# Optimization experiments

Hardware: AMD Instinct MI355X
Metric: run time of the kernel (lower is better)

The kernel has to match this reference:

```python
import jax, jax.numpy as jnp
import numpy as np
from jax import lax

N, CIN, COUT = 10000, 64, 32
RADIUS = 0.07
K = 32            # cap on neighbors per query (radius search truncated to K nearest)
KSIZE = 3         # kernel_size = [3,3,3]
NCELLS = KSIZE ** 3

# 8 trilinear corner offsets
_OFFS = np.array([[i, j, k] for i in (0, 1) for j in (0, 1) for k in (0, 1)], dtype=np.int32)  # (8,3)
_STRIDE = np.array([KSIZE * KSIZE, KSIZE, 1], dtype=np.int32)


def setup_inputs() -> dict:
    key = jax.random.key(0)
    k1, k2, k3 = jax.random.split(key, 3)
    points = jax.random.uniform(k1, (N, 3), dtype=jnp.float32)
    feats = jax.random.normal(k2, (N, CIN), dtype=jnp.float32)
    # ContinuousConv kernel: [3,3,3,Cin,Cout] flattened to [27,Cin,Cout]
    W = jax.random.normal(k3, (NCELLS, CIN, COUT), dtype=jnp.float32) * 0.05
    b = jnp.zeros((COUT,), dtype=jnp.float32)
    return {"feats": feats, "points": points, "W": W, "b": b}


def _neighbors(points):
    # squared pairwise distances (N,N); radius search truncated to K nearest
    sq = jnp.sum(points * points, axis=-1)
    d2 = sq[:, None] + sq[None, :] - 2.0 * (points @ points.T)
    neg_d2, idx = lax.top_k(-d2, K)           # (N,K)
    valid = (-neg_d2) <= RADIUS * RADIUS      # (N,K) bool
    return idx, valid


def _cconv(feats, points, W, b, idx, valid):
    nb_pos = points[idx]                      # (N,K,3) gather
    rel = (nb_pos - points[:, None, :]) / RADIUS   # normalized by half-extent -> unit ball
    # ball_to_cube_radial: v -> v * ||v||_2 / ||v||_inf  (0 at origin)
    l2 = jnp.linalg.norm(rel, axis=-1, keepdims=True)
    linf = jnp.max(jnp.abs(rel), axis=-1, keepdims=True)
    t = jnp.where(linf > 0, rel * (l2 / jnp.maximum(linf, 1e-12)), 0.0)  # in [-1,1]^3
    # map to kernel grid coords in [0, KSIZE-1]
    coords = (t + 1.0) * 0.5 * (KSIZE - 1)    # (N,K,3)
    c0 = jnp.clip(jnp.floor(coords), 0, KSIZE - 2)
    f = coords - c0                            # trilinear fractions, (N,K,3)
    offs = jnp.asarray(_OFFS)                  # (8,3)
    # trilinear weights (N,K,8)
    fw = jnp.where(offs[None, None] == 1, f[:, :, None, :], 1.0 - f[:, :, None, :])
    w8 = jnp.prod(fw, axis=-1)
    # flattened corner cell indices (N,K,8)
    cidx = jnp.sum((c0[:, :, None, :].astype(jnp.int32) + offs) * jnp.asarray(_STRIDE), axis=-1)
    onehot = jax.nn.one_hot(cidx, NCELLS, dtype=feats.dtype)        # (N,K,8,27)
    wmass = jnp.einsum('nke,nkej->nkj', w8, onehot)                 # (N,K,27)
    wmass = wmass * valid[:, :, None].astype(feats.dtype)
    nb_feats = feats[idx]                                           # (N,K,Cin)
    A = jnp.einsum('nkj,nkf->njf', wmass, nb_feats)                 # (N,27,Cin)
    out = jnp.einsum('njf,jfo->no', A, W)                           # (N,Cout)
    # normalize=True: divide by neighbor importance sum (count, window=None)
    nn = jnp.sum(valid.astype(feats.dtype), axis=-1)
    out = out / jnp.maximum(nn, 1.0)[:, None] + b
    return out


@jax.jit
def reference(feats, points, W, b):
    idx, valid = _neighbors(points)
    return _cconv(feats, points, W, b, idx, valid)
```

## Files before the change

kernel.cpp:

```cpp
#include <hip/hip_runtime.h>
#include <math.h>

#define N_PTS   10000
#define CIN     64
#define COUT    32
#define KCAP    32
#define RADIUSF 0.07f
#define NCELLS  27
#define QB      4
#define MAXC    48
#define GRES    14
#define GCELLS  (GRES * GRES * GRES)
#define CPAD    72
#define NBBLD   28
#define WT_ELEMS (NCELLS * COUT * CIN)

typedef __attribute__((ext_vector_type(8))) short         bf16x8_t;
typedef __attribute__((ext_vector_type(4))) float         f32x4_t;

__device__ __forceinline__ void cell_coords(float x, float y, float z,
                                            int& cx, int& cy, int& cz) {
    cx = (int)(x * (float)GRES); if (cx > GRES - 1) cx = GRES - 1; if (cx < 0) cx = 0;
    cy = (int)(y * (float)GRES); if (cy > GRES - 1) cy = GRES - 1; if (cy < 0) cy = 0;
    cz = (int)(z * (float)GRES); if (cz > GRES - 1) cz = GRES - 1; if (cz < 0) cz = 0;
}

__device__ __forceinline__ unsigned int f2bf_u(float x) {
    unsigned int u = __float_as_uint(x);
    return (u + 0x7FFFu + ((u >> 16) & 1u)) >> 16;
}

__global__ __launch_bounds__(1024) void build_rep_kernel(
    const float* __restrict__ pts,
    const float* __restrict__ W,
    int*   __restrict__ offsets,
    int*   __restrict__ sorted,
    int*   __restrict__ cursor,
    float* __restrict__ pts_s,
    unsigned short* __restrict__ Wt)
{
    __shared__ int   s_hist[GCELLS];
    __shared__ int   s_scan[1024];
    __shared__ float tile[CIN * 33];
    const int t = threadIdx.x;
    const int b = blockIdx.x;

    for (int i = t; i < GCELLS; i += 1024) s_hist[i] = 0;
    __syncthreads();
    for (int i = t; i < N_PTS; i += 1024) {
        int cx, cy, cz;
        cell_coords(pts[3 * i], pts[3 * i + 1], pts[3 * i + 2], cx, cy, cz);
        atomicAdd(&s_hist[(cx * GRES + cy) * GRES + cz], 1);
    }
    __syncthreads();

    const int c0 = t * 3;
    int v0 = (c0 + 0 < GCELLS) ? s_hist[c0 + 0] : 0;
    int v1 = (c0 + 1 < GCELLS) ? s_hist[c0 + 1] : 0;
    int v2 = (c0 + 2 < GCELLS) ? s_hist[c0 + 2] : 0;
    s_scan[t] = v0 + v1 + v2;
    __syncthreads();
    for (int d = 1; d < 1024; d <<= 1) {
        int add = (t >= d) ? s_scan[t - d] : 0;
        __syncthreads();
        s_scan[t] += add;
        __syncthreads();
    }
    int base = (t == 0) ? 0 : s_scan[t - 1];
    if (c0 + 0 < GCELLS) { s_hist[c0 + 0] = base; base += v0; }
    if (c0 + 1 < GCELLS) { s_hist[c0 + 1] = base; base += v1; }
    if (c0 + 2 < GCELLS) { s_hist[c0 + 2] = base; base += v2; }
    __syncthreads();

    if (b == 0) {
        for (int i = t; i < GCELLS; i += 1024) offsets[i] = s_hist[i];
        if (t == 0) offsets[GCELLS] = N_PTS;
    }

    const int per = (N_PTS + NBBLD - 1) / NBBLD;
    const int lo = b * per;
    const int hi = (lo + per < N_PTS) ? lo + per : N_PTS;
    for (int i = lo + t; i < hi; i += 1024) {
        float x = pts[3 * i + 0], y = pts[3 * i + 1], z = pts[3 * i + 2];
        int cx, cy, cz;
        cell_coords(x, y, z, cx, cy, cz);
        int cell = (cx * GRES + cy) * GRES + cz;
        int pos = s_hist[cell] + atomicAdd(&cursor[cell], 1);
        sorted[pos] = i;
        pts_s[3 * pos + 0] = x;
        pts_s[3 * pos + 1] = y;
        pts_s[3 * pos + 2] = z;
    }

    if (b >= 1) {
        const int cell = b - 1;
        __syncthreads();
        for (int idx = t; idx < CIN * COUT; idx += 1024) {
            int f = idx >> 5, o = idx & 31;
            tile[f * 33 + o] = W[cell * (CIN * COUT) + idx];
        }
        __syncthreads();
        for (int idx = t; idx < CIN * COUT; idx += 1024) {
            int o = idx >> 6, f = idx & 63;
            Wt[cell * (CIN * COUT) + idx] = (unsigned short)f2bf_u(tile[f * 33 + o]);
        }
    }
}

__global__ __launch_bounds__(256) void cconv_grid_mfma_kernel(
    const float* __restrict__ feats,
    const unsigned short* __restrict__ Wt,
    const float* __restrict__ bias,
    const int*   __restrict__ offsets,
    const int*   __restrict__ sorted,
    const float* __restrict__ pts_s,
    float* __restrict__ out)
{
    const int tid  = threadIdx.x;
    const int lane = tid & 63;
    const int wave = tid >> 6;

    __shared__ __align__(16) unsigned short sAb[QB][NCELLS][CPAD];
    __shared__ __align__(16) float s_pool[QB][4][MAXC];
    __shared__ int   s_idx[QB][MAXC];
    __shared__ int   s_sel[QB][KCAP];
    __shared__ int   s_cnt[QB];
    __shared__ int   s_qi[QB];
    __shared__ int   s_nn[QB];

    if (lane == 0) s_cnt[wave] = 0;

    const int q_flat = blockIdx.x * QB + wave;
    const int qi = sorted[q_flat];
    const float qx = pts_s[3 * q_flat + 0];
    const float qy = pts_s[3 * q_flat + 1];
    const float qz = pts_s[3 * q_flat + 2];
    const float sqn = qx * qx + qy * qy + qz * qz;
    const float r2 = RADIUSF * RADIUSF;

    int cx, cy, cz;
    cell_coords(qx, qy, qz, cx, cy, cz);

    int zlo = cz - 1; if (zlo < 0) zlo = 0;
    int zhi = cz + 1; if (zhi > GRES - 1) zhi = GRES - 1;
    int ss[9], sl[9];
    #pragma unroll
    for (int dxi = 0; dxi < 3; ++dxi) {
        #pragma unroll
        for (int dyi = 0; dyi < 3; ++dyi) {
            const int ii = dxi * 3 + dyi;
            int cxx = cx + dxi - 1, cyy = cy + dyi - 1;
            bool ok = (cxx >= 0) && (cxx <= GRES - 1) && (cyy >= 0) && (cyy <= GRES - 1);
            int row = ((ok ? cxx : 0) * GRES + (ok ? cyy : 0)) * GRES;
            int s = offsets[row + zlo];
            int e = offsets[row + zhi + 1];
            ss[ii] = s;
            sl[ii] = ok ? (e - s) : 0;
        }
    }
    int cum[10];
    cum[0] = 0;
    #pragma unroll
    for (int ii = 0; ii < 9; ++ii) cum[ii + 1] = cum[ii] + sl[ii];
    const int T = cum[9];

    for (int t = lane; t < T; t += 64) {
        int gidx = 0;
        #pragma unroll
        for (int ii = 0; ii < 9; ++ii) {
            bool in = (t >= cum[ii]) && (t < cum[ii + 1]);
            int cand = ss[ii] + (t - cum[ii]);
            gidx = in ? cand : gidx;
        }
        float x = pts_s[3 * gidx + 0];
        float y = pts_s[3 * gidx + 1];
        float z = pts_s[3 * gidx + 2];
        float sqj = x * x + y * y + z * z;
        float dot = qx * x + qy * y + qz * z;
        float d2 = (sqn + sqj) - 2.0f * dot;
        if (d2 <= r2) {
            int pos = atomicAdd(&s_cnt[wave], 1);
            if (pos < MAXC) {
                s_pool[wave][0][pos] = d2;
                s_pool[wave][1][pos] = x;
                s_pool[wave][2][pos] = y;
                s_pool[wave][3][pos] = z;
                s_idx[wave][pos] = sorted[gidx];
            }
        }
    }

    int M = s_cnt[wave]; if (M > MAXC) M = MAXC;
    const int cnt = (M > KCAP) ? KCAP : M;
    const bool over = (M > KCAP);

    if (over) {
        if (lane < M) {
            float dc = s_pool[wave][0][lane];
            int   ic = s_idx[wave][lane];
            int rank = 0;
            for (int m = 0; m < M; ++m) {
                float dm = s_pool[wave][0][m];
                int   im = s_idx[wave][m];
                rank += (dm < dc || (dm == dc && im < ic)) ? 1 : 0;
            }
            if (rank < KCAP) s_sel[wave][rank] = lane;
        }
    }
    if (lane == 0) { s_qi[wave] = qi; s_nn[wave] = cnt; }

    float* w9w = (float*)&sAb[wave][0][0];
    if (lane < cnt) {
        int slot = over ? s_sel[wave][lane] : lane;
        float x = s_pool[wave][1][slot];
        float y = s_pool[wave][2][slot];
        float z = s_pool[wave][3][slot];
        int   j = s_idx[wave][slot];
        float rx = (x - qx) / RADIUSF;
        float ry = (y - qy) / RADIUSF;
        float rz = (z - qz) / RADIUSF;
        float l2 = sqrtf(rx * rx + ry * ry + rz * rz);
        float ax = fabsf(rx), ay = fabsf(ry), az = fabsf(rz);
        float linf = fmaxf(fmaxf(ax, ay), az);
        float s = (linf > 0.0f) ? (l2 / fmaxf(linf, 1e-12f)) : 0.0f;
        float tx = rx * s, ty = ry * s, tz = rz * s;
        float cxf = (tx + 1.0f) * 0.5f * 2.0f;
        float cyf = (ty + 1.0f) * 0.5f * 2.0f;
        float czf = (tz + 1.0f) * 0.5f * 2.0f;
        float c0x = fminf(fmaxf(floorf(cxf), 0.0f), 1.0f);
        float c0y = fminf(fmaxf(floorf(cyf), 0.0f), 1.0f);
        float c0z = fminf(fmaxf(floorf(czf), 0.0f), 1.0f);
        float fx = cxf - c0x;
        float fy = cyf - c0y;
        float fz = czf - c0z;
        int i0 = (int)c0x, i1 = (int)c0y, i2 = (int)c0z;
        float gx0 = 1.0f - fx, gx1 = fx;
        float gy0 = 1.0f - fy, gy1 = fy;
        float gz0 = 1.0f - fz, gz1 = fz;
        float* wp = w9w + lane * 12;
        wp[0] = i0 ? 0.0f : gx0;  wp[1] = i0 ? gx0 : gx1;  wp[2] = i0 ? gx1 : 0.0f;
        wp[3] = i1 ? 0.0f : gy0;  wp[4] = i1 ? gy0 : gy1;  wp[5] = i1 ? gy1 : 0.0f;
        wp[6] = i2 ? 0.0f : gz0;  wp[7] = i2 ? gz0 : gz1;  wp[8] = i2 ? gz1 : 0.0f;
        wp[9] = __int_as_float(j * CIN);
    }

    float a[NCELLS];
    #pragma unroll
    for (int c = 0; c < NCELLS; ++c) a[c] = 0.0f;

    if (cnt > 0) {
        int jb = __float_as_int(w9w[9]);
        float fv = feats[jb + lane];
        for (int k = 0; k < cnt; ++k) {
            const float* wp = w9w + k * 12;
            float wxv[3] = {wp[0], wp[1], wp[2]};
            float wyv[3] = {wp[3], wp[4], wp[5]};
            float wz0 = wp[6], wz1 = wp[7], wz2 = wp[8];
            float fv_cur = fv;
            if (k + 1 < cnt) {
                int jb2 = __float_as_int(w9w[(k + 1) * 12 + 9]);
                fv = feats[jb2 + lane];
            }
            float pzv[3] = {wz0 * fv_cur, wz1 * fv_cur, wz2 * fv_cur};
            #pragma unroll
            for (int ci = 0; ci < 3; ++ci) {
                #pragma unroll
                for (int cj = 0; cj < 3; ++cj) {
                    float wxy = wxv[ci] * wyv[cj];
                    #pragma unroll
                    for (int ck = 0; ck < 3; ++ck) {
                        a[ci * 9 + cj * 3 + ck] = fmaf(wxy, pzv[ck], a[ci * 9 + cj * 3 + ck]);
                    }
                }
            }
        }
    }
    #pragma unroll
    for (int c = 0; c < NCELLS; ++c) sAb[wave][c][lane] = (unsigned short)f2bf_u(a[c]);
    __syncthreads();

    float (*sC)[QB][COUT] = (float (*)[QB][COUT])&s_pool[0][0][0];
    f32x4_t acc0 = {0.f, 0.f, 0.f, 0.f};
    f32x4_t acc1 = {0.f, 0.f, 0.f, 0.f};
    const int r  = lane & 15;
    const int kg = lane >> 4;
    for (int s = wave; s < 2 * NCELLS; s += QB) {
        const int c  = s >> 1;
        const int f0 = (s & 1) << 5;
        bf16x8_t af = {};
        if (r < QB) af = *(const bf16x8_t*)&sAb[r][c][f0 + kg * 8];
        const unsigned short* wp0 = Wt + ((c * COUT + r     ) * CIN + f0 + kg * 8);
        const unsigned short* wp1 = Wt + ((c * COUT + 16 + r) * CIN + f0 + kg * 8);
        bf16x8_t bf0 = *(const bf16x8_t*)wp0;
        bf16x8_t bf1 = *(const bf16x8_t*)wp1;
        acc0 = __builtin_amdgcn_mfma_f32_16x16x32_bf16(af, bf0, acc0, 0, 0, 0);
        acc1 = __builtin_amdgcn_mfma_f32_16x16x32_bf16(af, bf1, acc1, 0, 0, 0);
    }
    if (lane < 16) {
        #pragma unroll
        for (int j = 0; j < QB; ++j) {
            sC[wave][j][lane]      = acc0[j];
            sC[wave][j][16 + lane] = acc1[j];
        }
    }
    __syncthreads();

    if (tid < QB * COUT) {
        int q = tid >> 5, o = tid & 31;
        float v = sC[0][q][o] + sC[1][q][o] + sC[2][q][o] + sC[3][q][o];
        float nn = (float)s_nn[q];
        out[s_qi[q] * COUT + o] = v / fmaxf(nn, 1.0f) + bias[o];
    }
}

__global__ __launch_bounds__(64) void cconv_fused_kernel(
    const float* __restrict__ feats,
    const float* __restrict__ points,
    const float* __restrict__ W,
    const float* __restrict__ bias,
    float* __restrict__ out)
{
    const int n    = blockIdx.x;
    const int lane = threadIdx.x;

    __shared__ float sA[NCELLS][CIN];
    __shared__ float s_d2[128];
    __shared__ int   s_idx[128];
    __shared__ int   s_rank[128];
    __shared__ int   s_sel[KCAP];
    __shared__ int   s_cnt;

    if (lane == 0) s_cnt = 0;
    for (int c = lane; c < NCELLS * CIN; c += 64) ((float*)sA)[c] = 0.0f;
    __syncthreads();

    const float qx = points[3 * n + 0];
    const float qy = points[3 * n + 1];
    const float qz = points[3 * n + 2];
    const float sqn = qx * qx + qy * qy + qz * qz;
    const float r2 = RADIUSF * RADIUSF;

    for (int j = lane; j < N_PTS; j += 64) {
        float x = points[3 * j + 0];
        float y = points[3 * j + 1];
        float z = points[3 * j + 2];
        float sqj = x * x + y * y + z * z;
        float dot = qx * x + qy * y + qz * z;
        float d2 = (sqn + sqj) - 2.0f * dot;
        if (d2 <= r2) {
            int pos = atomicAdd(&s_cnt, 1);
            if (pos < 128) { s_d2[pos] = d2; s_idx[pos] = j; }
        }
    }
    __syncthreads();

    int M = s_cnt; if (M > 128) M = 128;
    int cnt;
    if (M > KCAP) {
        for (int c = lane; c < M; c += 64) {
            float dc = s_d2[c]; int ic = s_idx[c]; int rank = 0;
            for (int m = 0; m < M; ++m) {
                float dm = s_d2[m]; int im = s_idx[m];
                rank += (dm < dc || (dm == dc && im < ic)) ? 1 : 0;
            }
            s_rank[c] = rank;
        }
        __syncthreads();
        for (int c = lane; c < M; c += 64) {
            int r = s_rank[c];
            if (r < KCAP) s_sel[r] = s_idx[c];
        }
        __syncthreads();
        cnt = KCAP;
    } else cnt = M;
    const int* nbr = (M > KCAP) ? s_sel : s_idx;

    for (int k = 0; k < cnt; ++k) {
        int j = nbr[k];
        float x = points[3 * j + 0];
        float y = points[3 * j + 1];
        float z = points[3 * j + 2];
        float rx = (x - qx) / RADIUSF;
        float ry = (y - qy) / RADIUSF;
        float rz = (z - qz) / RADIUSF;
        float l2 = sqrtf(rx * rx + ry * ry + rz * rz);
        float ax = fabsf(rx), ay = fabsf(ry), az = fabsf(rz);
        float linf = fmaxf(fmaxf(ax, ay), az);
        float s = (linf > 0.0f) ? (l2 / fmaxf(linf, 1e-12f)) : 0.0f;
        float tx = rx * s, ty = ry * s, tz = rz * s;
        float cxf = (tx + 1.0f) * 0.5f * 2.0f;
        float cyf = (ty + 1.0f) * 0.5f * 2.0f;
        float czf = (tz + 1.0f) * 0.5f * 2.0f;
        float c0x = fminf(fmaxf(floorf(cxf), 0.0f), 1.0f);
        float c0y = fminf(fmaxf(floorf(cyf), 0.0f), 1.0f);
        float c0z = fminf(fmaxf(floorf(czf), 0.0f), 1.0f);
        float fx = cxf - c0x, fy = cyf - c0y, fz = czf - c0z;
        int i0 = (int)c0x, i1 = (int)c0y, i2 = (int)c0z;
        int base = i0 * 9 + i1 * 3 + i2;
        float gx0 = 1.0f - fx, gx1 = fx;
        float gy0 = 1.0f - fy, gy1 = fy;
        float gz0 = 1.0f - fz, gz1 = fz;
        float featv = feats[j * CIN + lane];
        sA[base + 0 ][lane] += (gx0 * gy0) * gz0 * featv;
        sA[base + 1 ][lane] += (gx0 * gy0) * gz1 * featv;
        sA[base + 3 ][lane] += (gx0 * gy1) * gz0 * featv;
        sA[base + 4 ][lane] += (gx0 * gy1) * gz1 * featv;
        sA[base + 9 ][lane] += (gx1 * gy0) * gz0 * featv;
        sA[base + 10][lane] += (gx1 * gy0) * gz1 * featv;
        sA[base + 12][lane] += (gx1 * gy1) * gz0 * featv;
        sA[base + 13][lane] += (gx1 * gy1) * gz1 * featv;
    }
    __syncthreads();

    const int o    = lane & 31;
    const int half = lane >> 5;
    const int c_begin = half ? 14 : 0;
    const int c_end   = half ? 27 : 14;
    float acc = 0.0f;
    for (int cell = c_begin; cell < c_end; ++cell) {
        const float* __restrict__ Wrow = W + (cell * CIN) * COUT + o;
        #pragma unroll 8
        for (int f = 0; f < CIN; ++f) acc += sA[cell][f] * Wrow[f * COUT];
    }
    acc += __shfl_xor(acc, 32);
    if (lane < COUT) {
        float nn = (float)cnt;
        out[n * COUT + lane] = acc / fmaxf(nn, 1.0f) + bias[lane];
    }
}

extern "C" void kernel_launch(void* const* d_in, const int* in_sizes, int n_in,
                              void* d_out, int out_size, void* d_ws, size_t ws_size,
                              hipStream_t stream) {
    const float* feats  = (const float*)d_in[0];
    const float* points = (const float*)d_in[1];
    const float* W      = (const float*)d_in[2];
    const float* bias   = (const float*)d_in[3];
    float* out = (float*)d_out;

    const size_t wt_bytes = (size_t)WT_ELEMS * sizeof(unsigned short);
    const size_t need     = wt_bytes
                          + (size_t)(GCELLS + 1 + N_PTS + GCELLS) * sizeof(int)
                          + (size_t)3 * N_PTS * sizeof(float);

    if (ws_size >= need) {
        unsigned short* Wt = (unsigned short*)d_ws;
        int* offsets = (int*)((char*)d_ws + wt_bytes);
        int* sorted  = offsets + GCELLS + 1;
        int* cursor  = sorted + N_PTS;
        float* pts_s = (float*)(cursor + GCELLS);

        hipMemsetAsync(cursor, 0, GCELLS * sizeof(int), stream);
        build_rep_kernel<<<NBBLD, 1024, 0, stream>>>(points, W, offsets, sorted, cursor, pts_s, Wt);
        cconv_grid_mfma_kernel<<<N_PTS / QB, QB * 64, 0, stream>>>(
            feats, Wt, bias, offsets, sorted, pts_s, out);
    } else {
        cconv_fused_kernel<<<N_PTS, 64, 0, stream>>>(feats, points, W, bias, out);
    }
}
```

Before: 120.8 us.

## Split grid build into single-block scan and scatter kernels; deepen feature prefetch

The redundant 28-block histogram-plus-scan becomes a single-block kernel with a wave-shuffle scan that writes the offsets and seeds the cursors. This removes the memset. A separate 256-thread kernel then does the point scatter across 40 blocks and the weight transpose across 27 blocks. In the conv kernel, the original-index lookup moves out of the candidate loop into a per-lane pass. Feature prefetch becomes two-deep, and the MFMA loop is fully unrolled to 14 iterations with a zero-padded extra cell row. This trades one extra kernel launch for less redundant work and serialization, and adds some shared memory.

```diff
diff --git a/kernel.cpp b/kernel.cpp
--- a/kernel.cpp
+++ b/kernel.cpp
@@ -12,7 +12,7 @@
 #define GRES    14
 #define GCELLS  (GRES * GRES * GRES)
 #define CPAD    72
-#define NBBLD   28
+#define NSCAT   40
 #define WT_ELEMS (NCELLS * COUT * CIN)
 
 typedef __attribute__((ext_vector_type(8))) short         bf16x8_t;
@@ -30,20 +30,16 @@
     return (u + 0x7FFFu + ((u >> 16) & 1u)) >> 16;
 }
 
-__global__ __launch_bounds__(1024) void build_rep_kernel(
+__global__ __launch_bounds__(1024) void k1_hist_scan(
     const float* __restrict__ pts,
-    const float* __restrict__ W,
-    int*   __restrict__ offsets,
-    int*   __restrict__ sorted,
-    int*   __restrict__ cursor,
-    float* __restrict__ pts_s,
-    unsigned short* __restrict__ Wt)
+    int* __restrict__ offsets,
+    int* __restrict__ cursor)
 {
-    __shared__ int   s_hist[GCELLS];
-    __shared__ int   s_scan[1024];
-    __shared__ float tile[CIN * 33];
+    __shared__ int s_hist[GCELLS];
+    __shared__ int s_wsum[16];
     const int t = threadIdx.x;
-    const int b = blockIdx.x;
+    const int lane = t & 63;
+    const int wv   = t >> 6;
 
     for (int i = t; i < GCELLS; i += 1024) s_hist[i] = 0;
     __syncthreads();
@@ -58,49 +54,63 @@
     int v0 = (c0 + 0 < GCELLS) ? s_hist[c0 + 0] : 0;
     int v1 = (c0 + 1 < GCELLS) ? s_hist[c0 + 1] : 0;
     int v2 = (c0 + 2 < GCELLS) ? s_hist[c0 + 2] : 0;
-    s_scan[t] = v0 + v1 + v2;
-    __syncthreads();
-    for (int d = 1; d < 1024; d <<= 1) {
-        int add = (t >= d) ? s_scan[t - d] : 0;
-        __syncthreads();
-        s_scan[t] += add;
-        __syncthreads();
-    }
-    int base = (t == 0) ? 0 : s_scan[t - 1];
-    if (c0 + 0 < GCELLS) { s_hist[c0 + 0] = base; base += v0; }
-    if (c0 + 1 < GCELLS) { s_hist[c0 + 1] = base; base += v1; }
-    if (c0 + 2 < GCELLS) { s_hist[c0 + 2] = base; base += v2; }
-    __syncthreads();
-
-    if (b == 0) {
-        for (int i = t; i < GCELLS; i += 1024) offsets[i] = s_hist[i];
-        if (t == 0) offsets[GCELLS] = N_PTS;
-    }
-
-    const int per = (N_PTS + NBBLD - 1) / NBBLD;
-    const int lo = b * per;
-    const int hi = (lo + per < N_PTS) ? lo + per : N_PTS;
-    for (int i = lo + t; i < hi; i += 1024) {
-        float x = pts[3 * i + 0], y = pts[3 * i + 1], z = pts[3 * i + 2];
-        int cx, cy, cz;
-        cell_coords(x, y, z, cx, cy, cz);
-        int cell = (cx * GRES + cy) * GRES + cz;
-        int pos = s_hist[cell] + atomicAdd(&cursor[cell], 1);
-        sorted[pos] = i;
-        pts_s[3 * pos + 0] = x;
-        pts_s[3 * pos + 1] = y;
-        pts_s[3 * pos + 2] = z;
-    }
-
-    if (b >= 1) {
-        const int cell = b - 1;
-        __syncthreads();
-        for (int idx = t; idx < CIN * COUT; idx += 1024) {
+    const int local = v0 + v1 + v2;
+    int inc = local;
+    #pragma unroll
+    for (int d = 1; d < 64; d <<= 1) {
+        int up = __shfl_up(inc, d);
+        if (lane >= d) inc += up;
+    }
+    if (lane == 63) s_wsum[wv] = inc;
+    __syncthreads();
+    if (t == 0) {
+        int run = 0;
+        #pragma unroll
+        for (int i = 0; i < 16; ++i) { int tmp = s_wsum[i]; s_wsum[i] = run; run += tmp; }
+    }
+    __syncthreads();
+    int base = s_wsum[wv] + (inc - local);
+    if (c0 + 0 < GCELLS) { offsets[c0 + 0] = base; cursor[c0 + 0] = base; base += v0; }
+    if (c0 + 1 < GCELLS) { offsets[c0 + 1] = base; cursor[c0 + 1] = base; base += v1; }
+    if (c0 + 2 < GCELLS) { offsets[c0 + 2] = base; cursor[c0 + 2] = base; base += v2; }
+    if (t == 0) offsets[GCELLS] = N_PTS;
+}
+
+__global__ __launch_bounds__(256) void k2_scatter_wt(
+    const float* __restrict__ pts,
+    const float* __restrict__ W,
+    int*   __restrict__ cursor,
+    int*   __restrict__ sorted,
+    float* __restrict__ pts_s,
+    unsigned short* __restrict__ Wt)
+{
+    const int b = blockIdx.x;
+    const int t = threadIdx.x;
+
+    if (b < NSCAT) {
+        const int per = N_PTS / NSCAT;
+        const int lo = b * per;
+        const int hi = lo + per;
+        for (int i = lo + t; i < hi; i += 256) {
+            float x = pts[3 * i + 0], y = pts[3 * i + 1], z = pts[3 * i + 2];
+            int cx, cy, cz;
+            cell_coords(x, y, z, cx, cy, cz);
+            int cell = (cx * GRES + cy) * GRES + cz;
+            int pos = atomicAdd(&cursor[cell], 1);
+            sorted[pos] = i;
+            pts_s[3 * pos + 0] = x;
+            pts_s[3 * pos + 1] = y;
+            pts_s[3 * pos + 2] = z;
+        }
+    } else {
+        __shared__ float tile[CIN * 33];
+        const int cell = b - NSCAT;
+        for (int idx = t; idx < CIN * COUT; idx += 256) {
             int f = idx >> 5, o = idx & 31;
             tile[f * 33 + o] = W[cell * (CIN * COUT) + idx];
         }
         __syncthreads();
-        for (int idx = t; idx < CIN * COUT; idx += 1024) {
+        for (int idx = t; idx < CIN * COUT; idx += 256) {
             int o = idx >> 6, f = idx & 63;
             Wt[cell * (CIN * COUT) + idx] = (unsigned short)f2bf_u(tile[f * 33 + o]);
         }
@@ -120,9 +130,10 @@
     const int lane = tid & 63;
     const int wave = tid >> 6;
 
-    __shared__ __align__(16) unsigned short sAb[QB][NCELLS][CPAD];
+    __shared__ __align__(16) unsigned short sAb[QB][NCELLS + 1][CPAD];
     __shared__ __align__(16) float s_pool[QB][4][MAXC];
     __shared__ int   s_idx[QB][MAXC];
+    __shared__ int   s_org[QB][MAXC];
     __shared__ int   s_sel[QB][KCAP];
     __shared__ int   s_cnt[QB];
     __shared__ int   s_qi[QB];
@@ -185,7 +196,7 @@
                 s_pool[wave][1][pos] = x;
                 s_pool[wave][2][pos] = y;
                 s_pool[wave][3][pos] = z;
-                s_idx[wave][pos] = sorted[gidx];
+                s_idx[wave][pos] = gidx;
             }
         }
     }
@@ -194,14 +205,16 @@
     const int cnt = (M > KCAP) ? KCAP : M;
     const bool over = (M > KCAP);
 
+    if (lane < M) s_org[wave][lane] = sorted[s_idx[wave][lane]];
+
     if (over) {
         if (lane < M) {
             float dc = s_pool[wave][0][lane];
-            int   ic = s_idx[wave][lane];
+            int   ic = s_org[wave][lane];
             int rank = 0;
             for (int m = 0; m < M; ++m) {
                 float dm = s_pool[wave][0][m];
-                int   im = s_idx[wave][m];
+                int   im = s_org[wave][m];
                 rank += (dm < dc || (dm == dc && im < ic)) ? 1 : 0;
             }
             if (rank < KCAP) s_sel[wave][rank] = lane;
@@ -215,7 +228,7 @@
         float x = s_pool[wave][1][slot];
         float y = s_pool[wave][2][slot];
         float z = s_pool[wave][3][slot];
-        int   j = s_idx[wave][slot];
+        int   j = s_org[wave][slot];
         float rx = (x - qx) / RADIUSF;
         float ry = (y - qy) / RADIUSF;
         float rz = (z - qz) / RADIUSF;
@@ -249,18 +262,17 @@
     for (int c = 0; c < NCELLS; ++c) a[c] = 0.0f;
 
     if (cnt > 0) {
-        int jb = __float_as_int(w9w[9]);
-        float fv = feats[jb + lane];
+        float fvA = feats[__float_as_int(w9w[9]) + lane];
+        float fvB = 0.0f;
+        if (cnt > 1) fvB = feats[__float_as_int(w9w[12 + 9]) + lane];
         for (int k = 0; k < cnt; ++k) {
             const float* wp = w9w + k * 12;
             float wxv[3] = {wp[0], wp[1], wp[2]};
             float wyv[3] = {wp[3], wp[4], wp[5]};
             float wz0 = wp[6], wz1 = wp[7], wz2 = wp[8];
-            float fv_cur = fv;
-            if (k + 1 < cnt) {
-                int jb2 = __float_as_int(w9w[(k + 1) * 12 + 9]);
-                fv = feats[jb2 + lane];
-            }
+            float fv_cur = fvA;
+            fvA = fvB;
+            if (k + 2 < cnt) fvB = feats[__float_as_int(w9w[(k + 2) * 12 + 9]) + lane];
             float pzv[3] = {wz0 * fv_cur, wz1 * fv_cur, wz2 * fv_cur};
             #pragma unroll
             for (int ci = 0; ci < 3; ++ci) {
@@ -277,6 +289,7 @@
     }
     #pragma unroll
     for (int c = 0; c < NCELLS; ++c) sAb[wave][c][lane] = (unsigned short)f2bf_u(a[c]);
+    sAb[wave][NCELLS][lane] = 0;
     __syncthreads();
 
     float (*sC)[QB][COUT] = (float (*)[QB][COUT])&s_pool[0][0][0];
@@ -284,13 +297,16 @@
     f32x4_t acc1 = {0.f, 0.f, 0.f, 0.f};
     const int r  = lane & 15;
     const int kg = lane >> 4;
-    for (int s = wave; s < 2 * NCELLS; s += QB) {
-        const int c  = s >> 1;
-        const int f0 = (s & 1) << 5;
+    #pragma unroll
+    for (int it = 0; it < 14; ++it) {
+        const int s5 = wave + it * 4;
+        const int c  = s5 >> 1;
+        const int f0 = (s5 & 1) << 5;
+        const int cw = (c < NCELLS) ? c : 0;
         bf16x8_t af = {};
         if (r < QB) af = *(const bf16x8_t*)&sAb[r][c][f0 + kg * 8];
-        const unsigned short* wp0 = Wt + ((c * COUT + r     ) * CIN + f0 + kg * 8);
-        const unsigned short* wp1 = Wt + ((c * COUT + 16 + r) * CIN + f0 + kg * 8);
+        const unsigned short* wp0 = Wt + ((cw * COUT + r     ) * CIN + f0 + kg * 8);
+        const unsigned short* wp1 = Wt + ((cw * COUT + 16 + r) * CIN + f0 + kg * 8);
         bf16x8_t bf0 = *(const bf16x8_t*)wp0;
         bf16x8_t bf1 = *(const bf16x8_t*)wp1;
         acc0 = __builtin_amdgcn_mfma_f32_16x16x32_bf16(af, bf0, acc0, 0, 0, 0);
@@ -440,18 +456,18 @@
 
     const size_t wt_bytes = (size_t)WT_ELEMS * sizeof(unsigned short);
     const size_t need     = wt_bytes
-                          + (size_t)(GCELLS + 1 + N_PTS + GCELLS) * sizeof(int)
+                          + (size_t)(GCELLS + 1 + GCELLS + N_PTS) * sizeof(int)
                           + (size_t)3 * N_PTS * sizeof(float);
 
     if (ws_size >= need) {
         unsigned short* Wt = (unsigned short*)d_ws;
         int* offsets = (int*)((char*)d_ws + wt_bytes);
-        int* sorted  = offsets + GCELLS + 1;
-        int* cursor  = sorted + N_PTS;
-        float* pts_s = (float*)(cursor + GCELLS);
-
-        hipMemsetAsync(cursor, 0, GCELLS * sizeof(int), stream);
-        build_rep_kernel<<<NBBLD, 1024, 0, stream>>>(points, W, offsets, sorted, cursor, pts_s, Wt);
+        int* cursor  = offsets + GCELLS + 1;
+        int* sorted  = cursor + GCELLS;
+        float* pts_s = (float*)(sorted + N_PTS);
+
+        k1_hist_scan<<<1, 1024, 0, stream>>>(points, offsets, cursor);
+        k2_scatter_wt<<<NSCAT + NCELLS, 256, 0, stream>>>(points, W, cursor, sorted, pts_s, Wt);
         cconv_grid_mfma_kernel<<<N_PTS / QB, QB * 64, 0, stream>>>(
             feats, Wt, bias, offsets, sorted, pts_s, out);
     } else {
```

Measured after the change: 115.3 us. -4.6%, faster.
